# Kernel optimization log

Measured on AMD Instinct MI355X. Metric: run time of the kernel, lower is better.

The kernel has to match this reference:

```python
import jax, jax.numpy as jnp
import numpy as np

N_SRC, N_MID, N_DST = 200000, 50000, 10000
D = 128
E1, E2 = 800000, 160000
EPS = 1e-12  # F.normalize eps


def setup_inputs() -> dict:
    key = jax.random.key(0)
    ks = jax.random.split(key, 12)
    s = 1.0 / np.sqrt(D)
    return {
        "x": jax.random.normal(ks[0], (N_SRC, D), jnp.float32),
        "W_l1": jax.random.uniform(ks[1], (D, D), jnp.float32, -s, s),
        "b_l1": jax.random.uniform(ks[2], (D,), jnp.float32, -s, s),
        "W_r1": jax.random.uniform(ks[3], (D, D), jnp.float32, -s, s),
        "W_l2": jax.random.uniform(ks[4], (D, D), jnp.float32, -s, s),
        "b_l2": jax.random.uniform(ks[5], (D,), jnp.float32, -s, s),
        "W_r2": jax.random.uniform(ks[6], (D, D), jnp.float32, -s, s),
        "row1": jax.random.randint(ks[7], (E1,), 0, N_SRC, jnp.int32),
        "col1": jax.random.randint(ks[8], (E1,), 0, N_MID, jnp.int32),
        "row2": jax.random.randint(ks[9], (E2,), 0, N_MID, jnp.int32),
        "col2": jax.random.randint(ks[10], (E2,), 0, N_DST, jnp.int32),
    }


def _sage_conv(x_src, x_dst, row, col, W_l, b_l, W_r, n_dst):
    # mean aggregation of source features over incoming edges (gather + scatter-add)
    msg = x_src[row]                                              # [E, D]
    agg = jax.ops.segment_sum(msg, col, num_segments=n_dst)       # [n_dst, D]
    deg = jax.ops.segment_sum(jnp.ones((row.shape[0],), x_src.dtype), col,
                              num_segments=n_dst)[:, None]        # [n_dst, 1]
    mean = jnp.where(deg > 0, agg / jnp.maximum(deg, 1.0), 0.0)
    out = mean @ W_l.T + b_l + x_dst @ W_r.T                      # lin_l + lin_r (root)
    # L2 normalize (normalize=True)
    norm = jnp.sqrt(jnp.sum(out * out, axis=-1, keepdims=True))
    return out / jnp.maximum(norm, EPS)


def reference(x, W_l1, b_l1, W_r1, W_l2, b_l2, W_r2, row1, col1, row2, col2):
    # layer 1: src = all sampled nodes, dst = first N_MID nodes
    h = _sage_conv(x, x[:N_MID], row1, col1, W_l1, b_l1, W_r1, N_MID)
    h = jax.nn.relu(h)  # dropout is identity in eval mode
    # layer 2: src = mid nodes, dst = first N_DST nodes (the batch targets)
    out = _sage_conv(h, h[:N_DST], row2, col2, W_l2, b_l2, W_r2, N_DST)
    return out
```

## Files before the change

### kernel.cpp

```cpp
#include <hip/hip_runtime.h>
#include <hip/hip_bf16.h>

#define DD 128
#define N_SRC 200000
#define N_MID 50000
#define N_DST 10000
#define E1 800000
#define E2 160000
#define CAP 64

typedef unsigned short u16;
typedef unsigned int u32;
typedef __attribute__((ext_vector_type(8))) short s16x8;
typedef __attribute__((ext_vector_type(4))) float f32x4;
typedef __attribute__((ext_vector_type(4))) int i32x4;
typedef __attribute__((ext_vector_type(4))) float fv4;


__device__ __forceinline__ float bf_lo(u32 u) {
    union { u32 u; float f; } v; v.u = u << 16; return v.f;
}
__device__ __forceinline__ float bf_hi(u32 u) {
    union { u32 u; float f; } v; v.u = u & 0xffff0000u; return v.f;
}
__device__ __forceinline__ u32 f2bf_bits(float f) {
    union { float f; u32 u; } v; v.f = f;
    return (v.u + 0x7fffu + ((v.u >> 16) & 1u)) >> 16;
}
__device__ __forceinline__ u32 pack2bf(float lo, float hi) {
    return f2bf_bits(lo) | (f2bf_bits(hi) << 16);
}


#define FILL1_SLICE  4000
#define FILL1_BLOCKS 1600
#define FILL2_SLICE  4000
#define FILL2_BLOCKS 320
#define FILL_BLOCKS  (FILL1_BLOCKS + FILL2_BLOCKS)

#define NCONV8 (N_SRC * DD / 8)
#define WTF_T 8192
#define PREP_T (NCONV8 + WTF_T)
#define PREP_BLOCKS ((PREP_T + 255) / 256)
#define PF_BLOCKS (FILL_BLOCKS + PREP_BLOCKS)

__global__ __launch_bounds__(256, 8) void prep_fill(
    const float* __restrict__ x, u16* __restrict__ xb,
    const float* __restrict__ Wl1, const float* __restrict__ Wr1,
    u16* __restrict__ WTf1,
    const float* __restrict__ Wl2, const float* __restrict__ Wr2,
    u16* __restrict__ WTf2,
    const int* __restrict__ row1, const int* __restrict__ col1,
    const int* __restrict__ row2, const int* __restrict__ col2,
    int* __restrict__ cnt1, int* __restrict__ cnt2,
    int* __restrict__ csr1, int* __restrict__ csr2)
{
    const int b = blockIdx.x;
    const int tid = threadIdx.x;

    if (b < FILL_BLOCKS) {
        const int* __restrict__ rowp;
        const int* __restrict__ colp;
        int* __restrict__ cnt;
        int* __restrict__ csr;
        int e0, e1, div;
        const int shard = b & 7;
        if (b < FILL1_BLOCKS) {
            int slice = b >> 3;
            e0 = slice * FILL1_SLICE; e1 = e0 + FILL1_SLICE;
            rowp = row1; colp = col1; cnt = cnt1; csr = csr1; div = 6250;
        } else {
            int slice = (b - FILL1_BLOCKS) >> 3;
            e0 = slice * FILL2_SLICE; e1 = e0 + FILL2_SLICE;
            rowp = row2; colp = col2; cnt = cnt2; csr = csr2; div = 1250;
        }
        const int lo = shard * div;
        for (int base = e0 + tid * 4; base < e1; base += 1024) {
            i32x4 c4 = __builtin_nontemporal_load((const i32x4*)(colp + base));
            i32x4 r4 = __builtin_nontemporal_load((const i32x4*)(rowp + base));
            #pragma unroll
            for (int k = 0; k < 4; ++k) {
                int c = c4[k];
                if ((u32)(c - lo) < (u32)div) {
                    int p = atomicAdd(&cnt[c], 1);
                    if (p < CAP) csr[(c << 6) + p] = r4[k];
                }
            }
        }
    } else {
        int i = (b - FILL_BLOCKS) * 256 + tid;
        if (i < NCONV8) {
            const fv4* x4 = (const fv4*)x;
            fv4 a = __builtin_nontemporal_load(x4 + i * 2);
            fv4 bb = __builtin_nontemporal_load(x4 + i * 2 + 1);
            uint4 o;
            o.x = pack2bf(a[0], a[1]); o.y = pack2bf(a[2], a[3]);
            o.z = pack2bf(bb[0], bb[1]); o.w = pack2bf(bb[2], bb[3]);
            ((uint4*)xb)[i] = o;
        } else if (i < NCONV8 + WTF_T) {
            int t = i - NCONV8;
            int layer = t >> 12;
            int rem = t & 4095;
            int kt = rem >> 9;
            int nt = (rem >> 6) & 7;
            int lane = rem & 63;
            int gn = nt * 16 + (lane & 15);
            int k0 = kt * 32 + (lane >> 4) * 8;
            const float* Wl = layer ? Wl2 : Wl1;
            const float* Wr = layer ? Wr2 : Wr1;
            u16* WTf = layer ? WTf2 : WTf1;
            u32 o[4];
            #pragma unroll
            for (int p = 0; p < 4; ++p) {
                int ka = k0 + 2 * p, kb = ka + 1;
                float ea = (ka < 128) ? Wl[gn * 128 + ka] : Wr[gn * 128 + (ka - 128)];
                float eb = (kb < 128) ? Wl[gn * 128 + kb] : Wr[gn * 128 + (kb - 128)];
                o[p] = pack2bf(ea, eb);
            }
            ((uint4*)WTf)[(kt * 8 + nt) * 64 + lane] = make_uint4(o[0], o[1], o[2], o[3]);
        }
    }
}


template <int ROWS, bool RELU, int MINB>
__global__ __launch_bounds__(256, MINB) void sage_kernel(
    const u16* __restrict__ xsrc_b, const u16* __restrict__ xdst_b,
    const int* __restrict__ cnt, const int* __restrict__ csrf,
    const u16* __restrict__ WTf, const float* __restrict__ bias,
    float* __restrict__ out_f, u16* __restrict__ out_b,
    int n_dst, int fp32lim)
{
    __shared__ float smem[ROWS * 132];
    const int tid = threadIdx.x;
    const int i0 = blockIdx.x * ROWS;
    const int lane = tid & 63;
    const int w = tid >> 6;
    const int quarter = lane >> 4;
    const int l16 = lane & 15;
    const int half = lane >> 5;
    const int l32 = lane & 31;
    constexpr int RPW = ROWS / 4;

    const uint4* __restrict__ xs4 = (const uint4*)xsrc_b;
    const uint2* __restrict__ xd2 = (const uint2*)xdst_b;
    uint4* sA4 = (uint4*)smem;
    uint2* sA2 = (uint2*)smem;

    for (int q = 0; q < RPW; ++q) {
        int r = w * RPW + q;
        int i = i0 + r;
        if (i < n_dst) {
            int deg = cnt[i];
            if (deg > CAP) deg = CAP;
            float acc[8] = {0.f, 0.f, 0.f, 0.f, 0.f, 0.f, 0.f, 0.f};
            if (deg > 0) {
                const int* bp = csrf + ((size_t)i << 6);
                int iv = bp[lane < deg ? lane : deg - 1];
                for (int g = 0; g < deg; g += 16) {
                    #pragma unroll
                    for (int j = 0; j < 4; ++j) {
                        if (g + 4 * j < deg) {
                            int rel = g + 4 * j + quarter;
                            int idx = __shfl(iv, rel & 63);
                            float m = (rel < deg) ? 1.f : 0.f;
                            uint4 u = xs4[(size_t)idx * 16 + l16];
                            acc[0] += m * bf_lo(u.x); acc[1] += m * bf_hi(u.x);
                            acc[2] += m * bf_lo(u.y); acc[3] += m * bf_hi(u.y);
                            acc[4] += m * bf_lo(u.z); acc[5] += m * bf_hi(u.z);
                            acc[6] += m * bf_lo(u.w); acc[7] += m * bf_hi(u.w);
                        }
                    }
                }
                #pragma unroll
                for (int k = 0; k < 8; ++k) {
                    acc[k] += __shfl_xor(acc[k], 16);
                    acc[k] += __shfl_xor(acc[k], 32);
                }
            }
            float s = (deg > 0) ? 1.f / (float)deg : 0.f;
            if (quarter == 0) {
                uint4 o;
                o.x = pack2bf(acc[0] * s, acc[1] * s);
                o.y = pack2bf(acc[2] * s, acc[3] * s);
                o.z = pack2bf(acc[4] * s, acc[5] * s);
                o.w = pack2bf(acc[6] * s, acc[7] * s);
                sA4[r * 33 + l16] = o;
            }
            if (half == 1) {
                sA2[r * 66 + 32 + l32] = xd2[(size_t)i * 32 + l32];
            }
        } else {
            if (quarter == 0) sA4[r * 33 + l16] = make_uint4(0, 0, 0, 0);
            if (half == 1)    sA2[r * 66 + 32 + l32] = make_uint2(0, 0);
        }
    }
    __syncthreads();

    constexpr int MT = ROWS / 16;
    const int nt0 = w * 2;
    const s16x8* sAv = (const s16x8*)smem;
    const s16x8* Bv = (const s16x8*)WTf;

    f32x4 C[MT][2];
    #pragma unroll
    for (int mt = 0; mt < MT; ++mt)
        #pragma unroll
        for (int ni = 0; ni < 2; ++ni)
            C[mt][ni] = (f32x4){0.f, 0.f, 0.f, 0.f};

    #pragma unroll
    for (int kt = 0; kt < 8; ++kt) {
        s16x8 a[MT];
        #pragma unroll
        for (int mt = 0; mt < MT; ++mt)
            a[mt] = sAv[(mt * 16 + l16) * 33 + kt * 4 + quarter];
        s16x8 b0 = Bv[(kt * 8 + nt0) * 64 + lane];
        s16x8 b1 = Bv[(kt * 8 + nt0 + 1) * 64 + lane];
        #pragma unroll
        for (int mt = 0; mt < MT; ++mt) {
            C[mt][0] = __builtin_amdgcn_mfma_f32_16x16x32_bf16(a[mt], b0, C[mt][0], 0, 0, 0);
            C[mt][1] = __builtin_amdgcn_mfma_f32_16x16x32_bf16(a[mt], b1, C[mt][1], 0, 0, 0);
        }
    }

    __syncthreads();
    float* sOut = smem;

    #pragma unroll
    for (int ni = 0; ni < 2; ++ni) {
        int col = (nt0 + ni) * 16 + l16;
        float bc = bias[col];
        #pragma unroll
        for (int mt = 0; mt < MT; ++mt) {
            #pragma unroll
            for (int r = 0; r < 4; ++r) {
                int row = mt * 16 + quarter * 4 + r;
                sOut[row * 132 + col] = C[mt][ni][r] + bc;
            }
        }
    }
    __syncthreads();

    constexpr int R = ROWS / 8;
    const int ty = tid >> 5;
    const int tx = tid & 31;
    #pragma unroll
    for (int r = 0; r < R; ++r) {
        int row = ty * R + r;
        float4 v = *(const float4*)(&sOut[row * 132 + tx * 4]);
        float s = v.x * v.x + v.y * v.y + v.z * v.z + v.w * v.w;
        #pragma unroll
        for (int off = 1; off < 32; off <<= 1) s += __shfl_xor(s, off);
        float scale = 1.f / fmaxf(sqrtf(s), 1e-12f);
        float v0 = v.x * scale, v1 = v.y * scale, v2 = v.z * scale, v3 = v.w * scale;
        if (RELU) {
            v0 = fmaxf(v0, 0.f); v1 = fmaxf(v1, 0.f);
            v2 = fmaxf(v2, 0.f); v3 = fmaxf(v3, 0.f);
        }
        int i = i0 + row;
        if (i < n_dst) {
            if (i < fp32lim)
                *(float4*)(out_f + (size_t)i * DD + tx * 4) = make_float4(v0, v1, v2, v3);
            if (out_b) {
                uint2 ob;
                ob.x = pack2bf(v0, v1);
                ob.y = pack2bf(v2, v3);
                *(uint2*)(out_b + (size_t)i * DD + tx * 4) = ob;
            }
        }
    }
}


extern "C" void kernel_launch(void* const* d_in, const int* in_sizes, int n_in,
                              void* d_out, int out_size, void* d_ws, size_t ws_size,
                              hipStream_t stream) {
    const float* x    = (const float*)d_in[0];
    const float* Wl1  = (const float*)d_in[1];
    const float* bl1  = (const float*)d_in[2];
    const float* Wr1  = (const float*)d_in[3];
    const float* Wl2  = (const float*)d_in[4];
    const float* bl2  = (const float*)d_in[5];
    const float* Wr2  = (const float*)d_in[6];
    const int* row1   = (const int*)d_in[7];
    const int* col1   = (const int*)d_in[8];
    const int* row2   = (const int*)d_in[9];
    const int* col2   = (const int*)d_in[10];
    float* out = (float*)d_out;

    char* p = (char*)d_ws;
    u16* xb    = (u16*)p;   p += (size_t)N_SRC * DD * sizeof(u16);
    u16* hb    = (u16*)p;   p += (size_t)N_MID * DD * sizeof(u16);
    u16* WTf1  = (u16*)p;   p += (size_t)256 * 128 * sizeof(u16);
    u16* WTf2  = (u16*)p;   p += (size_t)256 * 128 * sizeof(u16);
    int* cnt1  = (int*)p;   p += (size_t)(N_MID + 16) * sizeof(int);
    int* cnt2  = (int*)p;   p += (size_t)(N_DST + 16) * sizeof(int);
    int* csr1  = (int*)p;   p += (size_t)N_MID * CAP * sizeof(int);
    int* csr2  = (int*)p;   p += (size_t)N_DST * CAP * sizeof(int);

    hipMemsetAsync(cnt1, 0, (size_t)N_MID * sizeof(int), stream);
    hipMemsetAsync(cnt2, 0, (size_t)N_DST * sizeof(int), stream);

    prep_fill<<<PF_BLOCKS, 256, 0, stream>>>(
        x, xb, Wl1, Wr1, WTf1, Wl2, Wr2, WTf2,
        row1, col1, row2, col2, cnt1, cnt2, csr1, csr2);

    sage_kernel<32, true, 6><<<(N_MID + 31) / 32, 256, 0, stream>>>(
        xb, xb, cnt1, csr1, WTf1, bl1, (float*)nullptr, hb, N_MID, 0);

    sage_kernel<16, false, 6><<<(N_DST + 15) / 16, 256, 0, stream>>>(
        hb, hb, cnt2, csr2, WTf2, bl2, out, (u16*)nullptr, N_DST, N_DST);
}
```

Measured before the change: 276.7 us.

## Store per-node degree counter inside CSR bucket and drop separate count arrays

Moves each destination's atomic edge counter into slot 0 of its fixed-size neighbor bucket, so counting and neighbor writes share a cache line and the aggregation kernel reads degree and indices from one location. The fill loop now processes eight edges per thread per iteration, and the bf16 conversion of x uses nontemporal stores. In exchange, the whole CSR buffer must be zeroed each call instead of only small count arrays, and bucket capacity drops by one.

Result: slower. 358.5 us (+29.6%).

```diff
diff --git a/kernel.cpp b/kernel.cpp
--- a/kernel.cpp
+++ b/kernel.cpp
@@ -7,7 +7,7 @@
 #define N_DST 10000
 #define E1 800000
 #define E2 160000
-#define CAP 64
+#define BCAP 63
 
 typedef unsigned short u16;
 typedef unsigned int u32;
@@ -15,6 +15,7 @@
 typedef __attribute__((ext_vector_type(4))) float f32x4;
 typedef __attribute__((ext_vector_type(4))) int i32x4;
 typedef __attribute__((ext_vector_type(4))) float fv4;
+typedef __attribute__((ext_vector_type(4))) unsigned int u32x4;
 
 
 __device__ __forceinline__ float bf_lo(u32 u) {
@@ -52,7 +53,6 @@
     u16* __restrict__ WTf2,
     const int* __restrict__ row1, const int* __restrict__ col1,
     const int* __restrict__ row2, const int* __restrict__ col2,
-    int* __restrict__ cnt1, int* __restrict__ cnt2,
     int* __restrict__ csr1, int* __restrict__ csr2)
 {
     const int b = blockIdx.x;
@@ -61,29 +61,38 @@
     if (b < FILL_BLOCKS) {
         const int* __restrict__ rowp;
         const int* __restrict__ colp;
-        int* __restrict__ cnt;
         int* __restrict__ csr;
         int e0, e1, div;
         const int shard = b & 7;
         if (b < FILL1_BLOCKS) {
             int slice = b >> 3;
             e0 = slice * FILL1_SLICE; e1 = e0 + FILL1_SLICE;
-            rowp = row1; colp = col1; cnt = cnt1; csr = csr1; div = 6250;
+            rowp = row1; colp = col1; csr = csr1; div = 6250;
         } else {
             int slice = (b - FILL1_BLOCKS) >> 3;
             e0 = slice * FILL2_SLICE; e1 = e0 + FILL2_SLICE;
-            rowp = row2; colp = col2; cnt = cnt2; csr = csr2; div = 1250;
+            rowp = row2; colp = col2; csr = csr2; div = 1250;
         }
         const int lo = shard * div;
-        for (int base = e0 + tid * 4; base < e1; base += 1024) {
-            i32x4 c4 = __builtin_nontemporal_load((const i32x4*)(colp + base));
-            i32x4 r4 = __builtin_nontemporal_load((const i32x4*)(rowp + base));
+        for (int base = e0 + tid * 8; base < e1; base += 2048) {
+            i32x4 c4a = __builtin_nontemporal_load((const i32x4*)(colp + base));
+            i32x4 c4b = __builtin_nontemporal_load((const i32x4*)(colp + base + 4));
+            i32x4 r4a = __builtin_nontemporal_load((const i32x4*)(rowp + base));
+            i32x4 r4b = __builtin_nontemporal_load((const i32x4*)(rowp + base + 4));
             #pragma unroll
             for (int k = 0; k < 4; ++k) {
-                int c = c4[k];
+                int c = c4a[k];
                 if ((u32)(c - lo) < (u32)div) {
-                    int p = atomicAdd(&cnt[c], 1);
-                    if (p < CAP) csr[(c << 6) + p] = r4[k];
+                    int p = atomicAdd(csr + ((size_t)c << 6), 1);
+                    if (p < BCAP) csr[(c << 6) + 1 + p] = r4a[k];
+                }
+            }
+            #pragma unroll
+            for (int k = 0; k < 4; ++k) {
+                int c = c4b[k];
+                if ((u32)(c - lo) < (u32)div) {
+                    int p = atomicAdd(csr + ((size_t)c << 6), 1);
+                    if (p < BCAP) csr[(c << 6) + 1 + p] = r4b[k];
                 }
             }
         }
@@ -93,10 +102,10 @@
             const fv4* x4 = (const fv4*)x;
             fv4 a = __builtin_nontemporal_load(x4 + i * 2);
             fv4 bb = __builtin_nontemporal_load(x4 + i * 2 + 1);
-            uint4 o;
+            u32x4 o;
             o.x = pack2bf(a[0], a[1]); o.y = pack2bf(a[2], a[3]);
             o.z = pack2bf(bb[0], bb[1]); o.w = pack2bf(bb[2], bb[3]);
-            ((uint4*)xb)[i] = o;
+            __builtin_nontemporal_store(o, (u32x4*)xb + i);
         } else if (i < NCONV8 + WTF_T) {
             int t = i - NCONV8;
             int layer = t >> 12;
@@ -126,7 +135,7 @@
 template <int ROWS, bool RELU, int MINB>
 __global__ __launch_bounds__(256, MINB) void sage_kernel(
     const u16* __restrict__ xsrc_b, const u16* __restrict__ xdst_b,
-    const int* __restrict__ cnt, const int* __restrict__ csrf,
+    const int* __restrict__ csrf,
     const u16* __restrict__ WTf, const float* __restrict__ bias,
     float* __restrict__ out_f, u16* __restrict__ out_b,
     int n_dst, int fp32lim)
@@ -151,11 +160,12 @@
         int r = w * RPW + q;
         int i = i0 + r;
         if (i < n_dst) {
-            int deg = cnt[i];
-            if (deg > CAP) deg = CAP;
+            const int* bkt = csrf + ((size_t)i << 6);
+            int deg = bkt[0];
+            if (deg > BCAP) deg = BCAP;
             float acc[8] = {0.f, 0.f, 0.f, 0.f, 0.f, 0.f, 0.f, 0.f};
             if (deg > 0) {
-                const int* bp = csrf + ((size_t)i << 6);
+                const int* bp = bkt + 1;
                 int iv = bp[lane < deg ? lane : deg - 1];
                 for (int g = 0; g < deg; g += 16) {
                     #pragma unroll
@@ -294,21 +304,19 @@
     u16* hb    = (u16*)p;   p += (size_t)N_MID * DD * sizeof(u16);
     u16* WTf1  = (u16*)p;   p += (size_t)256 * 128 * sizeof(u16);
     u16* WTf2  = (u16*)p;   p += (size_t)256 * 128 * sizeof(u16);
-    int* cnt1  = (int*)p;   p += (size_t)(N_MID + 16) * sizeof(int);
-    int* cnt2  = (int*)p;   p += (size_t)(N_DST + 16) * sizeof(int);
-    int* csr1  = (int*)p;   p += (size_t)N_MID * CAP * sizeof(int);
-    int* csr2  = (int*)p;   p += (size_t)N_DST * CAP * sizeof(int);
-
-    hipMemsetAsync(cnt1, 0, (size_t)N_MID * sizeof(int), stream);
-    hipMemsetAsync(cnt2, 0, (size_t)N_DST * sizeof(int), stream);
+    int* csr1  = (int*)p;   p += (size_t)N_MID * 64 * sizeof(int);
+    int* csr2  = (int*)p;   p += (size_t)N_DST * 64 * sizeof(int);
+
+    (void)hipMemsetAsync(csr1, 0, (size_t)N_MID * 64 * sizeof(int), stream);
+    (void)hipMemsetAsync(csr2, 0, (size_t)N_DST * 64 * sizeof(int), stream);
 
     prep_fill<<<PF_BLOCKS, 256, 0, stream>>>(
         x, xb, Wl1, Wr1, WTf1, Wl2, Wr2, WTf2,
-        row1, col1, row2, col2, cnt1, cnt2, csr1, csr2);
+        row1, col1, row2, col2, csr1, csr2);
 
     sage_kernel<32, true, 6><<<(N_MID + 31) / 32, 256, 0, stream>>>(
-        xb, xb, cnt1, csr1, WTf1, bl1, (float*)nullptr, hb, N_MID, 0);
+        xb, xb, csr1, WTf1, bl1, (float*)nullptr, hb, N_MID, 0);
 
     sage_kernel<16, false, 6><<<(N_DST + 15) / 16, 256, 0, stream>>>(
-        hb, hb, cnt2, csr2, WTf2, bl2, out, (u16*)nullptr, N_DST, N_DST);
-}
+        hb, hb, csr2, WTf2, bl2, out, (u16*)nullptr, N_DST, N_DST);
+}
```
